# Kernel optimization log

Hardware: AMD Instinct MI355X
Metric: run time of the kernel (lower is better)

The kernel has to match this reference:

```python
import jax, jax.numpy as jnp
import numpy as np
from jax.scipy.special import logsumexp

B, T, D, H, K = 64, 800, 80, 128, 39  # batch, frames, feat dim, LSTM hidden/dir, num phones


def setup_inputs() -> dict:
    key = jax.random.key(0)
    ks = jax.random.split(key, 16)
    s = 0.1
    inp = {
        "features": jax.random.normal(ks[0], (B, T, D), jnp.float32),
        "lengths": jax.random.randint(ks[1], (B,), T // 2, T + 1, dtype=jnp.int32),
        "labels": jax.random.randint(ks[2], (B, T), 0, K, dtype=jnp.int32),
        # BiLSTM params (PyTorch layout: W_ih (4H,D), W_hh (4H,H); gate order i,f,g,o)
        "Wih_f": jax.random.normal(ks[3], (4 * H, D), jnp.float32) * s,
        "Whh_f": jax.random.normal(ks[4], (4 * H, H), jnp.float32) * s,
        "bih_f": jax.random.normal(ks[5], (4 * H,), jnp.float32) * s,
        "bhh_f": jax.random.normal(ks[6], (4 * H,), jnp.float32) * s,
        "Wih_b": jax.random.normal(ks[7], (4 * H, D), jnp.float32) * s,
        "Whh_b": jax.random.normal(ks[8], (4 * H, H), jnp.float32) * s,
        "bih_b": jax.random.normal(ks[9], (4 * H,), jnp.float32) * s,
        "bhh_b": jax.random.normal(ks[10], (4 * H,), jnp.float32) * s,
        # emission projection Linear(2H -> K)
        "Wp": jax.random.normal(ks[11], (K, 2 * H), jnp.float32) * s,
        "bp": jax.random.normal(ks[12], (K,), jnp.float32) * s,
        # CRF params (pytorch-crf init: U(-0.1, 0.1))
        "start_t": jax.random.uniform(ks[13], (K,), jnp.float32, -0.1, 0.1),
        "end_t": jax.random.uniform(ks[14], (K,), jnp.float32, -0.1, 0.1),
        "trans": jax.random.uniform(ks[15], (K, K), jnp.float32, -0.1, 0.1),
    }
    return inp


def _lstm(x, Wih, Whh, bih, bhh, reverse):
    """Single-direction LSTM over padded batch. x: (B,T,D) -> (B,T,H)."""
    nB, nT, _ = x.shape
    nH = Whh.shape[1]
    xW = jnp.swapaxes(x @ Wih.T + (bih + bhh), 0, 1)  # (T,B,4H)

    def step(carry, g):
        h, c = carry
        g = g + h @ Whh.T
        i, f, gg, o = jnp.split(g, 4, axis=-1)
        c = jax.nn.sigmoid(f) * c + jax.nn.sigmoid(i) * jnp.tanh(gg)
        h = jax.nn.sigmoid(o) * jnp.tanh(c)
        return (h, c), h

    init = (jnp.zeros((nB, nH), x.dtype), jnp.zeros((nB, nH), x.dtype))
    _, hs = jax.lax.scan(step, init, xW, reverse=reverse)
    return jnp.swapaxes(hs, 0, 1)  # (B,T,H)


def _crf_nll(emissions, labels, lengths, start_t, end_t, trans):
    """pytorch-crf: -mean log-likelihood. emissions (B,T,K), labels (B,T)."""
    nB, nT, nK = emissions.shape
    mask = (jnp.arange(nT)[None, :] < lengths[:, None])  # (B,T)
    mf = mask.astype(emissions.dtype)
    bidx = jnp.arange(nB)

    # --- numerator: score of gold path ---
    num = start_t[labels[:, 0]] + emissions[bidx, 0, labels[:, 0]]
    tr = trans[labels[:, :-1], labels[:, 1:]]  # (B,T-1)
    em = jnp.take_along_axis(emissions[:, 1:], labels[:, 1:, None], axis=2)[..., 0]
    num = num + ((tr + em) * mf[:, 1:]).sum(axis=1)
    last_tags = jnp.take_along_axis(labels, (lengths - 1)[:, None], axis=1)[:, 0]
    num = num + end_t[last_tags]

    # --- denominator: forward algorithm ---
    alpha0 = start_t[None, :] + emissions[:, 0]  # (B,K)
    em_rest = jnp.swapaxes(emissions[:, 1:], 0, 1)  # (T-1,B,K)
    m_rest = jnp.swapaxes(mask[:, 1:], 0, 1)  # (T-1,B)

    def step(alpha, inputs):
        em_t, m_t = inputs
        nxt = logsumexp(alpha[:, :, None] + trans[None] + em_t[:, None, :], axis=1)
        return jnp.where(m_t[:, None], nxt, alpha), None

    alpha, _ = jax.lax.scan(step, alpha0, (em_rest, m_rest))
    denom = logsumexp(alpha + end_t[None, :], axis=1)

    return -(num - denom).mean()


def reference(features, lengths, labels, Wih_f, Whh_f, bih_f, bhh_f,
              Wih_b, Whh_b, bih_b, bhh_b, Wp, bp, start_t, end_t, trans):
    h_f = _lstm(features, Wih_f, Whh_f, bih_f, bhh_f, reverse=False)
    h_b = _lstm(features, Wih_b, Whh_b, bih_b, bhh_b, reverse=True)
    hidden = jnp.concatenate([h_f, h_b], axis=-1)  # (B,T,2H)
    emissions = hidden @ Wp.T + bp  # (B,T,K)
    return _crf_nll(emissions, labels, lengths, start_t, end_t, trans)
```

## Files before the change

### kernel.cpp

```cpp
#include <hip/hip_runtime.h>
#include <cstddef>
#include <cstdint>

#define B_ 64
#define T_ 800
#define D_ 80
#define H_ 128
#define K_ 39
#define BT_ (B_ * T_)

#define NL2E_  (-1.44269504f)
#define N2L2E_ (-2.88539008f)

typedef _Float16 h2_t  __attribute__((ext_vector_type(2)));
typedef _Float16 f16x8 __attribute__((ext_vector_type(8)));
typedef float    f32x4 __attribute__((ext_vector_type(4)));
typedef uint32_t u32x4 __attribute__((ext_vector_type(4)));

__device__ __forceinline__ float fdot2_(h2_t a, h2_t b, float c) {
#if __has_builtin(__builtin_amdgcn_fdot2)
  return __builtin_amdgcn_fdot2(a, b, c, false);
#else
  return c + (float)a.x * (float)b.x + (float)a.y * (float)b.y;
#endif
}

__device__ __forceinline__ h2_t asH2u_(uint32_t u) { return __builtin_bit_cast(h2_t, u); }

__device__ __forceinline__ float ex2_(float x) {
#if __has_builtin(__builtin_amdgcn_exp2f)
  return __builtin_amdgcn_exp2f(x);
#else
  return __builtin_exp2f(x);
#endif
}
__device__ __forceinline__ float rcpf_(float x) {
#if __has_builtin(__builtin_amdgcn_rcpf)
  return __builtin_amdgcn_rcpf(x);
#else
  return 1.0f / x;
#endif
}
__device__ __forceinline__ float tanhf_(float x) { return 2.0f / (1.0f + __expf(-2.0f * x)) - 1.0f; }

__device__ __forceinline__ float laneb_(float v, int lane) {
  return __builtin_bit_cast(float, __builtin_amdgcn_readlane(__builtin_bit_cast(int, v), lane));
}
__device__ __forceinline__ uint32_t lanebu_(uint32_t v, int lane) {
  return (uint32_t)__builtin_amdgcn_readlane((int)v, lane);
}

__device__ __forceinline__ float dppswap1_(float v) {
  return __builtin_bit_cast(float,
    __builtin_amdgcn_mov_dpp(__builtin_bit_cast(int, v), 0xB1, 0xF, 0xF, true));
}

template<int CTRL>
__device__ __forceinline__ uint32_t dppu_(uint32_t v) {
  return (uint32_t)__builtin_amdgcn_mov_dpp((int)v, CTRL, 0xF, 0xF, true);
}

__device__ __forceinline__ void barrier_lds_() {
  asm volatile("s_waitcnt lgkmcnt(0)" ::: "memory");
  __builtin_amdgcn_s_barrier();
}

__device__ __forceinline__ void rows_of_(int tid, int& unit, int& role, int& r0, int& r1) {
  const int w = tid >> 6, L = tid & 63;
  unit = w * 32 + (L >> 1);
  role = L & 1;
  r0 = role * H_ + unit;
  r1 = 2 * H_ + role * H_ + unit;
}

__global__ __launch_bounds__(256, 1)
void xw_kernel(const float* __restrict__ x,
               const float* __restrict__ Wih_f, const float* __restrict__ Wih_b,
               _Float16* __restrict__ xw)
{
  const int dir = blockIdx.x & 1;
  const int mc  = blockIdx.x >> 1;
  const float* W = dir ? Wih_b : Wih_f;

  const int tid  = threadIdx.x;
  const int w    = tid >> 6;
  const int lane = tid & 63;
  const int lm   = lane & 15;
  const int quad = lane >> 4;
  const int selw = w >> 1;
  const int rolw = w & 1;

  f16x8 Bf[8][3];
  #pragma unroll
  for (int nt = 0; nt < 8; ++nt) {
    const int r = w * 128 + nt * 16 + lm;
    const float fac = (r >= 256 && r < 384) ? N2L2E_ : NL2E_;
    #pragma unroll
    for (int kt = 0; kt < 3; ++kt) {
      const int kb = kt * 32 + quad * 8;
      #pragma unroll
      for (int j = 0; j < 8; ++j) {
        const int k = kb + j;
        Bf[nt][kt][j] = (k < D_) ? (_Float16)(fac * W[(size_t)r * D_ + k]) : (_Float16)0.0f;
      }
    }
  }

  __shared__ alignas(16) _Float16 xs[128 * 96];
  for (int i = tid; i < 128 * 96; i += 256) xs[i] = (_Float16)0.0f;

  for (int cc = 0; cc < 4; ++cc) {
    const int base = mc * 512 + cc * 128;
    __syncthreads();
    {
      const float4* src = (const float4*)(x + (size_t)base * D_);
      for (int i = tid; i < 128 * D_ / 4; i += 256) {
        float4 v = src[i];
        const int row = i / 20, col = (i % 20) * 4;
        h2_t p0, p1;
        p0.x = (_Float16)v.x; p0.y = (_Float16)v.y;
        p1.x = (_Float16)v.z; p1.y = (_Float16)v.w;
        uint2 pk;
        pk.x = __builtin_bit_cast(uint32_t, p0);
        pk.y = __builtin_bit_cast(uint32_t, p1);
        *(uint2*)&xs[row * 96 + col] = pk;
      }
    }
    __syncthreads();

    #pragma unroll
    for (int mt = 0; mt < 8; ++mt) {
      f16x8 Af[3];
      #pragma unroll
      for (int kt = 0; kt < 3; ++kt)
        Af[kt] = *(const f16x8*)&xs[(mt * 16 + lm) * 96 + kt * 32 + quad * 8];

      f32x4 acc[8];
      #pragma unroll
      for (int nt = 0; nt < 8; ++nt) acc[nt] = (f32x4){0.f, 0.f, 0.f, 0.f};
      #pragma unroll
      for (int kt = 0; kt < 3; ++kt)
        #pragma unroll
        for (int nt = 0; nt < 8; ++nt)
          acc[nt] = __builtin_amdgcn_mfma_f32_16x16x32_f16(Af[kt], Bf[nt][kt], acc[nt], 0, 0, 0);

      #pragma unroll
      for (int nt = 0; nt < 8; ++nt) {
        const int unit = nt * 16 + lm;
        const int ptid = (unit >> 5) * 64 + (unit & 31) * 2 + rolw;
        #pragma unroll
        for (int rg = 0; rg < 4; ++rg) {
          const int bt = base + mt * 16 + quad * 4 + rg;
          xw[((size_t)dir * BT_ + bt) * 512 + ptid * 2 + selw] = (_Float16)acc[nt][rg];
        }
      }
    }
  }
}

template<int USE_XW>
__global__ __launch_bounds__(256, 1)
void lstm_kernel(const float* __restrict__ x,
                 const float* __restrict__ Wih_f, const float* __restrict__ Whh_f,
                 const float* __restrict__ bih_f, const float* __restrict__ bhh_f,
                 const float* __restrict__ Wih_b, const float* __restrict__ Whh_b,
                 const float* __restrict__ bih_b, const float* __restrict__ bhh_b,
                 const _Float16* __restrict__ xw,
                 _Float16* __restrict__ hcat)
{
  const int bb  = blockIdx.x & 63;
  const int dir = blockIdx.x >> 6;
  const float* Whh = dir ? Whh_b : Whh_f;
  const float* Wih = dir ? Wih_b : Wih_f;
  const float* bih = dir ? bih_b : bih_f;
  const float* bhh = dir ? bhh_b : bhh_f;

  const int tid  = threadIdx.x;
  const int lane = tid & 63;
  const int Q    = lane & 3;
  int unit, role, r0, r1; rows_of_(tid, unit, role, r0, r1);
  const float s0 = NL2E_;
  const float s1 = role ? NL2E_ : N2L2E_;
  const float qk2 = role ? 0.0f : -1.0f;

  h2_t wp0[64], wp1[64];
  #pragma unroll
  for (int r = 0; r < 4; ++r) {
    const int ch = Q ^ r;
    #pragma unroll
    for (int jj = 0; jj < 16; ++jj) {
      const int j = ch * 16 + jj;
      float2 a = *(const float2*)(Whh + (size_t)r0 * H_ + 2 * j);
      float2 d = *(const float2*)(Whh + (size_t)r1 * H_ + 2 * j);
      wp0[r * 16 + jj].x = (_Float16)(s0 * a.x); wp0[r * 16 + jj].y = (_Float16)(s0 * a.y);
      wp1[r * 16 + jj].x = (_Float16)(s1 * d.x); wp1[r * 16 + jj].y = (_Float16)(s1 * d.y);
    }
  }
  h2_t wx0[40], wx1[40];
  if (!USE_XW) {
    #pragma unroll
    for (int i = 0; i < 40; ++i) {
      float2 a = *(const float2*)(Wih + (size_t)r0 * D_ + 2 * i);
      float2 d = *(const float2*)(Wih + (size_t)r1 * D_ + 2 * i);
      wx0[i].x = (_Float16)(s0 * a.x); wx0[i].y = (_Float16)(s0 * a.y);
      wx1[i].x = (_Float16)(s1 * d.x); wx1[i].y = (_Float16)(s1 * d.y);
    }
  }
  const float bias0 = s0 * (bih[r0] + bhh[r0]);
  const float bias1 = s1 * (bih[r1] + bhh[r1]);

  __shared__ alignas(16) _Float16 hsf[2][H_];
  __shared__ uint32_t xs2[2][64];

  if (tid < H_) hsf[0][tid] = (_Float16)0.0f;
  if (!USE_XW && tid < 64) { xs2[0][tid] = 0u; xs2[1][tid] = 0u; }
  float c = 0.0f;

  const uint32_t* xwdu = (const uint32_t*)xw + ((size_t)dir * BT_ + (size_t)bb * T_) * 256;
  const float*    xb   = x + (size_t)bb * T_ * D_;
  _Float16*       hb   = hcat + (size_t)bb * T_ * (2 * H_) + dir * H_;

  _Float16* hbp = hb + (size_t)(dir ? (T_ - 1) : 0) * (2 * H_);
  const ptrdiff_t hstep = dir ? -(2 * H_) : (2 * H_);
  int xoff = (dir ? (T_ - 3) : 2) * 256 + tid;
  const int xstep = dir ? -256 : 256;

  uint32_t xwA = 0u, xwB = 0u;
  h2_t xpend; xpend.x = (_Float16)0.f; xpend.y = (_Float16)0.f;
  {
    const int tq0 = dir ? (T_ - 1) : 0;
    const int tq1 = dir ? (T_ - 2) : 1;
    if (USE_XW) {
      xwA = xwdu[(size_t)tq0 * 256 + tid];
      xwB = xwdu[(size_t)tq1 * 256 + tid];
    } else if (tid < 40) {
      float2 v0 = *(const float2*)(xb + (size_t)tq0 * D_ + 2 * tid);
      h2_t p; p.x = (_Float16)v0.x; p.y = (_Float16)v0.y;
      xs2[0][tid] = __builtin_bit_cast(uint32_t, p);
      float2 v1 = *(const float2*)(xb + (size_t)tq1 * D_ + 2 * tid);
      xpend.x = (_Float16)v1.x; xpend.y = (_Float16)v1.y;
    }
  }
  __syncthreads();

  auto step = [&](int tt, int par, uint32_t& xwreg) {
    float a[4], b[4];
    if (USE_XW) {
      const h2_t xv = asH2u_(xwreg);
      a[0] = bias0 + (float)xv.x;
      b[0] = bias1 + (float)xv.y;
      a[1] = a[2] = a[3] = 0.f; b[1] = b[2] = b[3] = 0.f;
      xwreg = xwdu[xoff];
    } else {
      a[0] = bias0; b[0] = bias1;
      a[1] = a[2] = a[3] = 0.f; b[1] = b[2] = b[3] = 0.f;
      if (tid < 40) {
        xs2[par ^ 1][tid] = __builtin_bit_cast(uint32_t, xpend);
        const int ttc = (tt + 2 < T_) ? (tt + 2) : (T_ - 1);
        const int tq2 = dir ? (T_ - 1 - ttc) : ttc;
        float2 v = *(const float2*)(xb + (size_t)tq2 * D_ + 2 * tid);
        xpend.x = (_Float16)v.x; xpend.y = (_Float16)v.y;
      }
      uint32_t xreg = xs2[par][lane];
      #pragma unroll
      for (int j = 0; j < 40; j += 4) {
        h2_t q0 = asH2u_(lanebu_(xreg, j));
        h2_t q1 = asH2u_(lanebu_(xreg, j + 1));
        h2_t q2 = asH2u_(lanebu_(xreg, j + 2));
        h2_t q3 = asH2u_(lanebu_(xreg, j + 3));
        a[0] = fdot2_(wx0[j],     q0, a[0]); b[0] = fdot2_(wx1[j],     q0, b[0]);
        a[1] = fdot2_(wx0[j + 1], q1, a[1]); b[1] = fdot2_(wx1[j + 1], q1, b[1]);
        a[2] = fdot2_(wx0[j + 2], q2, a[2]); b[2] = fdot2_(wx1[j + 2], q2, b[2]);
        a[3] = fdot2_(wx0[j + 3], q3, a[3]); b[3] = fdot2_(wx1[j + 3], q3, b[3]);
      }
    }

    const u32x4* hq = (const u32x4*)hsf[par];
    u32x4 ovr[4];
    #pragma unroll
    for (int reg = 0; reg < 4; ++reg) ovr[reg] = hq[Q * 4 + reg];

    u32x4 x1[4], x2[4], x3[4];
    #pragma unroll
    for (int reg = 0; reg < 4; ++reg) {
      #pragma unroll
      for (int e = 0; e < 4; ++e) {
        x1[reg][e] = dppu_<0xB1>(ovr[reg][e]);
        x2[reg][e] = dppu_<0x4E>(ovr[reg][e]);
        x3[reg][e] = dppu_<0x1B>(ovr[reg][e]);
      }
    }

    #define HROUND_(HV, RB)                                        \
      _Pragma("unroll")                                            \
      for (int reg = 0; reg < 4; ++reg) {                          \
        _Pragma("unroll")                                          \
        for (int e = 0; e < 4; ++e) {                              \
          const h2_t hh = asH2u_((HV)[reg][e]);                    \
          a[e] = fdot2_(wp0[(RB) + reg * 4 + e], hh, a[e]);        \
          b[e] = fdot2_(wp1[(RB) + reg * 4 + e], hh, b[e]);        \
        }                                                          \
      }
    HROUND_(ovr, 0)
    HROUND_(x1, 16)
    HROUND_(x2, 32)
    HROUND_(x3, 48)
    #undef HROUND_

    const float ga = (a[0] + a[1]) + (a[2] + a[3]);
    const float gb = (b[0] + b[1]) + (b[2] + b[3]);

    const float ea = ex2_(ga);
    const float sg = rcpf_(1.0f + ea);
    const float gbc = fminf(fmaxf(gb, -34.6f), 34.6f);
    const float eb = ex2_(gbc);
    const float qv = fmaf(qk2, eb, 1.0f) * rcpf_(1.0f + eb);
    const float ex = dppswap1_(sg * qv);
    c = fmaf(sg, c, ex);
    const float hn = qv * tanhf_(c);
    if (role) {
      hsf[par ^ 1][unit] = (_Float16)hn;
      hbp[unit] = (_Float16)hn;
    }
    hbp += hstep;
    if (tt + 3 < T_) xoff += xstep;
    barrier_lds_();
  };

  for (int tb = 0; tb < T_; tb += 2) {
    step(tb,     0, xwA);
    step(tb + 1, 1, xwB);
  }
}

__global__ __launch_bounds__(256, 1)
void emis_kernel(const _Float16* __restrict__ hcat,
                 const float* __restrict__ Wp, const float* __restrict__ bp,
                 float* __restrict__ em)
{
  const int tid  = threadIdx.x;
  const int w    = tid >> 6;
  const int lane = tid & 63;
  const int lm   = lane & 15;
  const int quad = lane >> 4;

  f16x8 Bf[3][8];
  float bias[3];
  #pragma unroll
  for (int nt = 0; nt < 3; ++nt) {
    const int n = nt * 16 + lm;
    const bool valid = n < K_;
    bias[nt] = valid ? bp[n] : 0.0f;
    #pragma unroll
    for (int kt = 0; kt < 8; ++kt) {
      const int kb = kt * 32 + quad * 8;
      #pragma unroll
      for (int j = 0; j < 8; ++j)
        Bf[nt][kt][j] = valid ? (_Float16)Wp[(size_t)n * 256 + kb + j] : (_Float16)0.0f;
    }
  }

  #pragma unroll
  for (int q = 0; q < 4; ++q) {
    const int mt  = blockIdx.x * 16 + w * 4 + q;
    const int bt0 = mt * 16;

    f16x8 Af[8];
    const _Float16* ab = hcat + ((size_t)bt0 + lm) * 256;
    #pragma unroll
    for (int kt = 0; kt < 8; ++kt)
      Af[kt] = *(const f16x8*)(ab + kt * 32 + quad * 8);

    f32x4 acc[3];
    #pragma unroll
    for (int nt = 0; nt < 3; ++nt) acc[nt] = (f32x4){0.f, 0.f, 0.f, 0.f};
    #pragma unroll
    for (int kt = 0; kt < 8; ++kt)
      #pragma unroll
      for (int nt = 0; nt < 3; ++nt)
        acc[nt] = __builtin_amdgcn_mfma_f32_16x16x32_f16(Af[kt], Bf[nt][kt], acc[nt], 0, 0, 0);

    #pragma unroll
    for (int nt = 0; nt < 3; ++nt) {
      const int n = nt * 16 + lm;
      if (n < K_) {
        #pragma unroll
        for (int rg = 0; rg < 4; ++rg) {
          const int row = bt0 + quad * 4 + rg;
          em[(size_t)row * K_ + n] = acc[nt][rg] + bias[nt];
        }
      }
    }
  }
}

__global__ __launch_bounds__(256)
void crf_dn_kernel(const float* __restrict__ em,
                   const int* __restrict__ labels, const int* __restrict__ lengths,
                   const float* __restrict__ start_t, const float* __restrict__ end_t,
                   const float* __restrict__ trans,
                   float* __restrict__ dn)
{
  const int b    = blockIdx.x;
  const int tid  = threadIdx.x;
  const int wv   = tid >> 6;
  const int lane = tid & 63;
  const int len  = lengths[b];
  const float* emb = em + (size_t)b * T_ * K_;

  __shared__ float s_num[3];
  __shared__ float s_den;

  if (wv == 0) {
    float et[K_];
    #pragma unroll
    for (int j = 0; j < K_; ++j)
      et[j] = (lane < K_) ? __expf(trans[j * K_ + lane]) : 0.0f;

    float a0 = (lane < K_) ? (start_t[lane] + emb[lane]) : -1e30f;
    float m = a0;
    #pragma unroll
    for (int off = 32; off > 0; off >>= 1) m = fmaxf(m, __shfl_xor(m, off));
    float v = __expf(a0 - m);
    float off_acc = m;

    auto ldc = [&](int t) -> float {
      const int tc = (t < len) ? t : (len - 1);
      return (lane < K_) ? emb[(size_t)tc * K_ + lane] : 0.0f;
    };

    float eA = ldc(1), eB = ldc(2), eC = ldc(3), eD = ldc(4);
    float eE = ldc(5), eF = ldc(6), eG = ldc(7), eH = ldc(8);

    auto stepden = [&](float& ereg, int tt) {
      const float emc = ereg;
      ereg = ldc(tt + 8);
      if (tt < len) {
        const float pv = v;
        float s0 = 0.f, s1 = 0.f, s2 = 0.f, s3 = 0.f;
        #pragma unroll
        for (int j = 0; j < 36; j += 4) {
          s0 = fmaf(laneb_(pv, j),     et[j],     s0);
          s1 = fmaf(laneb_(pv, j + 1), et[j + 1], s1);
          s2 = fmaf(laneb_(pv, j + 2), et[j + 2], s2);
          s3 = fmaf(laneb_(pv, j + 3), et[j + 3], s3);
        }
        s0 = fmaf(laneb_(pv, 36), et[36], s0);
        s1 = fmaf(laneb_(pv, 37), et[37], s1);
        s2 = fmaf(laneb_(pv, 38), et[38], s2);
        v = ((s0 + s1) + (s2 + s3)) * __expf(emc);
        if ((tt & 1) == 0) {
          const float sc = laneb_(v, 0);
          v *= 1.0f / sc;
          off_acc += __logf(sc);
        }
      }
    };

    for (int t = 1; t < len; t += 8) {
      stepden(eA, t);     stepden(eB, t + 1);
      stepden(eC, t + 2); stepden(eD, t + 3);
      stepden(eE, t + 4); stepden(eF, t + 5);
      stepden(eG, t + 6); stepden(eH, t + 7);
    }

    float w = (lane < K_) ? v * __expf(end_t[lane]) : 0.0f;
    #pragma unroll
    for (int off = 32; off > 0; off >>= 1) w += __shfl_xor(w, off);
    if (lane == 0) s_den = off_acc + __logf(w);
  } else {
    const int idx = tid - 64;
    float acc = 0.0f;
    for (int t = 1 + idx; t < len; t += 192) {
      const int lp = labels[b * T_ + t - 1];
      const int lc = labels[b * T_ + t];
      acc += trans[lp * K_ + lc] + emb[(size_t)t * K_ + lc];
    }
    if (tid == 64) {
      const int l0 = labels[b * T_];
      const int ll = labels[b * T_ + len - 1];
      acc += start_t[l0] + emb[l0] + end_t[ll];
    }
    #pragma unroll
    for (int off = 32; off > 0; off >>= 1) acc += __shfl_xor(acc, off);
    if (lane == 0) s_num[wv - 1] = acc;
  }
  __syncthreads();
  if (tid == 0) dn[b] = s_den - (s_num[0] + s_num[1] + s_num[2]);
}

__global__ void finalize_kernel(const float* __restrict__ dn, float* __restrict__ out)
{
  const int tid = threadIdx.x;
  float v = dn[tid];
  #pragma unroll
  for (int off = 32; off > 0; off >>= 1) v += __shfl_down(v, off);
  if (tid == 0) out[0] = v * (1.0f / 64.0f);
}

extern "C" void kernel_launch(void* const* d_in, const int* in_sizes, int n_in,
                              void* d_out, int out_size, void* d_ws, size_t ws_size,
                              hipStream_t stream)
{
  (void)in_sizes; (void)n_in; (void)out_size;
  const float* features = (const float*)d_in[0];
  const int*   lengths  = (const int*)d_in[1];
  const int*   labels   = (const int*)d_in[2];
  const float* Wih_f = (const float*)d_in[3];
  const float* Whh_f = (const float*)d_in[4];
  const float* bih_f = (const float*)d_in[5];
  const float* bhh_f = (const float*)d_in[6];
  const float* Wih_b = (const float*)d_in[7];
  const float* Whh_b = (const float*)d_in[8];
  const float* bih_b = (const float*)d_in[9];
  const float* bhh_b = (const float*)d_in[10];
  const float* Wp      = (const float*)d_in[11];
  const float* bp      = (const float*)d_in[12];
  const float* start_t = (const float*)d_in[13];
  const float* end_t   = (const float*)d_in[14];
  const float* trans   = (const float*)d_in[15];
  float* out = (float*)d_out;

  char* wsc = (char*)d_ws;
  _Float16* hcatH = (_Float16*)wsc;
  float*    em    = (float*)(wsc + 26214400);
  float*    dn    = (float*)(wsc + 26214400 + 7987200);
  _Float16* xwH   = (_Float16*)(wsc + 34202112);
  const bool big  = ws_size >= (size_t)34202112 + 104857600;

  if (big) {
    hipLaunchKernelGGL(xw_kernel, dim3(200), dim3(256), 0, stream,
                       features, Wih_f, Wih_b, xwH);
    hipLaunchKernelGGL((lstm_kernel<1>), dim3(2 * B_), dim3(256), 0, stream,
                       features, Wih_f, Whh_f, bih_f, bhh_f,
                       Wih_b, Whh_b, bih_b, bhh_b, xwH, hcatH);
  } else {
    hipLaunchKernelGGL((lstm_kernel<0>), dim3(2 * B_), dim3(256), 0, stream,
                       features, Wih_f, Whh_f, bih_f, bhh_f,
                       Wih_b, Whh_b, bih_b, bhh_b, xwH, hcatH);
  }
  hipLaunchKernelGGL(emis_kernel, dim3(BT_ / 256), dim3(256), 0, stream,
                     hcatH, Wp, bp, em);
  hipLaunchKernelGGL(crf_dn_kernel, dim3(B_), dim3(256), 0, stream,
                     em, labels, lengths, start_t, end_t, trans, dn);
  hipLaunchKernelGGL(finalize_kernel, dim3(1), dim3(64), 0, stream,
                     dn, out);
}
```

Baseline: 749.0 us.

## Switch LSTM recurrent matvec from fp16 dot2 to fp32 packed FMA

The recurrent Whh weights are now held as fp32 pairs in registers and the hidden state is shared through LDS as fp32. The h·W product uses v_pk_fma_f32 in place of fp16 fdot2. This doubles LDS reads and DPP shuffles per step and roughly doubles weight register footprint (256 VGPRs of weights), risking spills. Accuracy improves, and any speed gain depends on packed-FMA throughput compared with fdot2.

```diff
diff --git a/kernel.cpp b/kernel.cpp
--- a/kernel.cpp
+++ b/kernel.cpp
@@ -15,6 +15,7 @@
 typedef _Float16 h2_t  __attribute__((ext_vector_type(2)));
 typedef _Float16 f16x8 __attribute__((ext_vector_type(8)));
 typedef float    f32x4 __attribute__((ext_vector_type(4)));
+typedef float    f32x2 __attribute__((ext_vector_type(2)));
 typedef uint32_t u32x4 __attribute__((ext_vector_type(4)));
 
 __device__ __forceinline__ float fdot2_(h2_t a, h2_t b, float c) {
@@ -58,6 +59,17 @@
 template<int CTRL>
 __device__ __forceinline__ uint32_t dppu_(uint32_t v) {
   return (uint32_t)__builtin_amdgcn_mov_dpp((int)v, CTRL, 0xF, 0xF, true);
+}
+
+__device__ __forceinline__ void pkfma_(f32x2& acc, f32x2 a, f32x2 b) {
+  asm("v_pk_fma_f32 %0, %1, %2, %0" : "+v"(acc) : "v"(a), "v"(b));
+}
+
+__device__ __forceinline__ f32x2 mkf2_(uint32_t lo, uint32_t hi) {
+  f32x2 r;
+  r.x = __builtin_bit_cast(float, lo);
+  r.y = __builtin_bit_cast(float, hi);
+  return r;
 }
 
 __device__ __forceinline__ void barrier_lds_() {
@@ -183,17 +195,17 @@
   const float s1 = role ? NL2E_ : N2L2E_;
   const float qk2 = role ? 0.0f : -1.0f;
 
-  h2_t wp0[64], wp1[64];
+  f32x2 wp0f[64], wp1f[64];
   #pragma unroll
   for (int r = 0; r < 4; ++r) {
     const int ch = Q ^ r;
     #pragma unroll
-    for (int jj = 0; jj < 16; ++jj) {
-      const int j = ch * 16 + jj;
-      float2 a = *(const float2*)(Whh + (size_t)r0 * H_ + 2 * j);
-      float2 d = *(const float2*)(Whh + (size_t)r1 * H_ + 2 * j);
-      wp0[r * 16 + jj].x = (_Float16)(s0 * a.x); wp0[r * 16 + jj].y = (_Float16)(s0 * a.y);
-      wp1[r * 16 + jj].x = (_Float16)(s1 * d.x); wp1[r * 16 + jj].y = (_Float16)(s1 * d.y);
+    for (int m = 0; m < 16; ++m) {
+      const int j = 32 * ch + 2 * m;
+      float2 a = *(const float2*)(Whh + (size_t)r0 * H_ + j);
+      float2 d = *(const float2*)(Whh + (size_t)r1 * H_ + j);
+      wp0f[r * 16 + m].x = s0 * a.x; wp0f[r * 16 + m].y = s0 * a.y;
+      wp1f[r * 16 + m].x = s1 * d.x; wp1f[r * 16 + m].y = s1 * d.y;
     }
   }
   h2_t wx0[40], wx1[40];
@@ -209,10 +221,10 @@
   const float bias0 = s0 * (bih[r0] + bhh[r0]);
   const float bias1 = s1 * (bih[r1] + bhh[r1]);
 
-  __shared__ alignas(16) _Float16 hsf[2][H_];
+  __shared__ alignas(16) float hsf32[2][H_];
   __shared__ uint32_t xs2[2][64];
 
-  if (tid < H_) hsf[0][tid] = (_Float16)0.0f;
+  if (tid < H_) hsf32[0][tid] = 0.0f;
   if (!USE_XW && tid < 64) { xs2[0][tid] = 0u; xs2[1][tid] = 0u; }
   float c = 0.0f;
 
@@ -244,16 +256,13 @@
   __syncthreads();
 
   auto step = [&](int tt, int par, uint32_t& xwreg) {
-    float a[4], b[4];
+    float xa = bias0, xb0 = bias1;
     if (USE_XW) {
       const h2_t xv = asH2u_(xwreg);
-      a[0] = bias0 + (float)xv.x;
-      b[0] = bias1 + (float)xv.y;
-      a[1] = a[2] = a[3] = 0.f; b[1] = b[2] = b[3] = 0.f;
+      xa  += (float)xv.x;
+      xb0 += (float)xv.y;
       xwreg = xwdu[xoff];
     } else {
-      a[0] = bias0; b[0] = bias1;
-      a[1] = a[2] = a[3] = 0.f; b[1] = b[2] = b[3] = 0.f;
       if (tid < 40) {
         xs2[par ^ 1][tid] = __builtin_bit_cast(uint32_t, xpend);
         const int ttc = (tt + 2 < T_) ? (tt + 2) : (T_ - 1);
@@ -262,53 +271,58 @@
         xpend.x = (_Float16)v.x; xpend.y = (_Float16)v.y;
       }
       uint32_t xreg = xs2[par][lane];
-      #pragma unroll
-      for (int j = 0; j < 40; j += 4) {
+      float x1a = 0.f, x1b = 0.f;
+      #pragma unroll
+      for (int j = 0; j < 40; j += 2) {
         h2_t q0 = asH2u_(lanebu_(xreg, j));
         h2_t q1 = asH2u_(lanebu_(xreg, j + 1));
-        h2_t q2 = asH2u_(lanebu_(xreg, j + 2));
-        h2_t q3 = asH2u_(lanebu_(xreg, j + 3));
-        a[0] = fdot2_(wx0[j],     q0, a[0]); b[0] = fdot2_(wx1[j],     q0, b[0]);
-        a[1] = fdot2_(wx0[j + 1], q1, a[1]); b[1] = fdot2_(wx1[j + 1], q1, b[1]);
-        a[2] = fdot2_(wx0[j + 2], q2, a[2]); b[2] = fdot2_(wx1[j + 2], q2, b[2]);
-        a[3] = fdot2_(wx0[j + 3], q3, a[3]); b[3] = fdot2_(wx1[j + 3], q3, b[3]);
-      }
-    }
-
-    const u32x4* hq = (const u32x4*)hsf[par];
-    u32x4 ovr[4];
-    #pragma unroll
-    for (int reg = 0; reg < 4; ++reg) ovr[reg] = hq[Q * 4 + reg];
-
-    u32x4 x1[4], x2[4], x3[4];
-    #pragma unroll
-    for (int reg = 0; reg < 4; ++reg) {
-      #pragma unroll
-      for (int e = 0; e < 4; ++e) {
-        x1[reg][e] = dppu_<0xB1>(ovr[reg][e]);
-        x2[reg][e] = dppu_<0x4E>(ovr[reg][e]);
-        x3[reg][e] = dppu_<0x1B>(ovr[reg][e]);
-      }
-    }
-
-    #define HROUND_(HV, RB)                                        \
-      _Pragma("unroll")                                            \
-      for (int reg = 0; reg < 4; ++reg) {                          \
-        _Pragma("unroll")                                          \
-        for (int e = 0; e < 4; ++e) {                              \
-          const h2_t hh = asH2u_((HV)[reg][e]);                    \
-          a[e] = fdot2_(wp0[(RB) + reg * 4 + e], hh, a[e]);        \
-          b[e] = fdot2_(wp1[(RB) + reg * 4 + e], hh, b[e]);        \
-        }                                                          \
-      }
-    HROUND_(ovr, 0)
-    HROUND_(x1, 16)
-    HROUND_(x2, 32)
-    HROUND_(x3, 48)
-    #undef HROUND_
-
-    const float ga = (a[0] + a[1]) + (a[2] + a[3]);
-    const float gb = (b[0] + b[1]) + (b[2] + b[3]);
+        xa  = fdot2_(wx0[j],     q0, xa);  xb0 = fdot2_(wx1[j],     q0, xb0);
+        x1a = fdot2_(wx0[j + 1], q1, x1a); x1b = fdot2_(wx1[j + 1], q1, x1b);
+      }
+      xa += x1a; xb0 += x1b;
+    }
+
+    const u32x4* hq = (const u32x4*)hsf32[par];
+    u32x4 ch[8];
+    #pragma unroll
+    for (int g = 0; g < 8; ++g) ch[g] = hq[Q * 8 + g];
+
+    f32x2 A[4], Bv[4];
+    #pragma unroll
+    for (int e = 0; e < 4; ++e) { A[e].x = 0.f; A[e].y = 0.f; Bv[e].x = 0.f; Bv[e].y = 0.f; }
+
+    #define HR_(CHV, RB)                                            \
+      _Pragma("unroll")                                             \
+      for (int m = 0; m < 16; ++m) {                                \
+        const f32x2 hh = mkf2_((CHV)[m >> 1][(m & 1) * 2],          \
+                               (CHV)[m >> 1][(m & 1) * 2 + 1]);     \
+        pkfma_(A[m & 3],  wp0f[(RB) + m], hh);                      \
+        pkfma_(Bv[m & 3], wp1f[(RB) + m], hh);                      \
+      }
+
+    HR_(ch, 0)
+    u32x4 cx[8];
+    #pragma unroll
+    for (int g = 0; g < 8; ++g)
+      #pragma unroll
+      for (int e = 0; e < 4; ++e) cx[g][e] = dppu_<0xB1>(ch[g][e]);
+    HR_(cx, 16)
+    #pragma unroll
+    for (int g = 0; g < 8; ++g)
+      #pragma unroll
+      for (int e = 0; e < 4; ++e) cx[g][e] = dppu_<0x4E>(ch[g][e]);
+    HR_(cx, 32)
+    #pragma unroll
+    for (int g = 0; g < 8; ++g)
+      #pragma unroll
+      for (int e = 0; e < 4; ++e) cx[g][e] = dppu_<0x1B>(ch[g][e]);
+    HR_(cx, 48)
+    #undef HR_
+
+    const float ga = xa  + ((A[0].x + A[0].y) + (A[1].x + A[1].y))
+                         + ((A[2].x + A[2].y) + (A[3].x + A[3].y));
+    const float gb = xb0 + ((Bv[0].x + Bv[0].y) + (Bv[1].x + Bv[1].y))
+                         + ((Bv[2].x + Bv[2].y) + (Bv[3].x + Bv[3].y));
 
     const float ea = ex2_(ga);
     const float sg = rcpf_(1.0f + ea);
@@ -319,7 +333,7 @@
     c = fmaf(sg, c, ex);
     const float hn = qv * tanhf_(c);
     if (role) {
-      hsf[par ^ 1][unit] = (_Float16)hn;
+      hsf32[par ^ 1][unit] = hn;
       hbp[unit] = (_Float16)hn;
     }
     hbp += hstep;
```

Measured after the change: 1.019 ms. 36.0% more time.
